# Kernel tuning notes

Hardware: AMD Instinct MI355X
Metric: run time of the kernel (lower is better)

The kernel has to match this reference:

```python
import jax, jax.numpy as jnp
import numpy as np

N_NODES = 50000
N_EDGES = 800000
IN_C = 116
HEADS = 4
OUT_C = 16
OUT_DIM = HEADS * OUT_C  # 64
NUM_GRAPHS = 100
NEG_SLOPE = 0.2
BN_EPS = 1e-5


def setup_inputs() -> dict:
    key = jax.random.key(0)
    ks = jax.random.split(key, 16)
    x = jax.random.normal(ks[0], (N_NODES, IN_C), dtype=jnp.float32)
    edge_index = jax.random.randint(ks[1], (2, N_EDGES), 0, N_NODES, dtype=jnp.int32)
    edge_attr = jax.random.normal(ks[2], (N_EDGES, 1), dtype=jnp.float32)
    batch = jnp.sort(jax.random.randint(ks[3], (N_NODES,), 0, NUM_GRAPHS, dtype=jnp.int32))
    s = 0.1
    return {
        "x": x, "edge_index": edge_index, "edge_attr": edge_attr, "batch": batch,
        "Wl": jax.random.normal(ks[4], (IN_C, OUT_DIM)) * s,
        "bl": jnp.zeros((OUT_DIM,), jnp.float32),
        "Wr": jax.random.normal(ks[5], (IN_C, OUT_DIM)) * s,
        "br": jnp.zeros((OUT_DIM,), jnp.float32),
        "We": jax.random.normal(ks[6], (1, OUT_DIM)) * s,
        "att": jax.random.normal(ks[7], (HEADS, OUT_C)) * s,
        "gat_bias": jnp.zeros((OUT_DIM,), jnp.float32),
        "gamma": jnp.ones((OUT_DIM,), jnp.float32),
        "beta": jnp.zeros((OUT_DIM,), jnp.float32),
        "Wres": jax.random.normal(ks[8], (IN_C, OUT_DIM)) * s,
        "bres": jnp.zeros((OUT_DIM,), jnp.float32),
        "W1": jax.random.normal(ks[9], (OUT_DIM, 64)) * s,
        "b1": jnp.zeros((64,), jnp.float32),
        "W2": jax.random.normal(ks[10], (64, 2)) * s,
        "b2": jnp.zeros((2,), jnp.float32),
    }


def _gatv2(x, edge_index, edge_attr, Wl, bl, Wr, br, We, att, gat_bias):
    N = x.shape[0]
    # linear transforms (PyG lin_l applies to source/message, lin_r to target)
    xl = (x @ Wl + bl).reshape(N, HEADS, OUT_C)
    xr = (x @ Wr + br).reshape(N, HEADS, OUT_C)
    # add self loops with fill_value=1.0 for edge_attr
    loops = jnp.arange(N, dtype=edge_index.dtype)
    src = jnp.concatenate([edge_index[0], loops])
    dst = jnp.concatenate([edge_index[1], loops])
    ea = jnp.concatenate([edge_attr, jnp.ones((N, 1), edge_attr.dtype)], axis=0)
    edge_emb = (ea @ We).reshape(-1, HEADS, OUT_C)          # [E+N, H, C]
    # GATv2 scores: att . leaky_relu(xl_j + xr_i + edge_emb)
    e = jax.nn.leaky_relu(xl[src] + xr[dst] + edge_emb, NEG_SLOPE)
    logits = jnp.einsum('ehc,hc->eh', e, att)                # [E+N, H]
    # segment softmax over incoming edges of each target node
    m = jax.ops.segment_max(logits, dst, num_segments=N)     # [N, H]
    ex = jnp.exp(logits - m[dst])
    denom = jax.ops.segment_sum(ex, dst, num_segments=N)     # [N, H]
    alpha = ex / denom[dst]
    # weighted scatter-add of source messages
    out = jax.ops.segment_sum(alpha[:, :, None] * xl[src], dst, num_segments=N)
    return out.reshape(N, OUT_DIM) + gat_bias


def reference(x, edge_index, edge_attr, batch, Wl, bl, Wr, br, We, att, gat_bias,
              gamma, beta, Wres, bres, W1, b1, W2, b2):
    h = _gatv2(x, edge_index, edge_attr, Wl, bl, Wr, br, We, att, gat_bias)
    # BatchNorm1d (training-style batch statistics over node dim)
    mu = jnp.mean(h, axis=0)
    var = jnp.var(h, axis=0)
    h = gamma * (h - mu) * jax.lax.rsqrt(var + BN_EPS) + beta
    # residual projection of original features
    h = h + (x @ Wres + bres)
    # global mean pool per graph
    sums = jax.ops.segment_sum(h, batch, num_segments=NUM_GRAPHS)
    cnts = jax.ops.segment_sum(jnp.ones((h.shape[0],), h.dtype), batch, num_segments=NUM_GRAPHS)
    pooled = sums / jnp.maximum(cnts, 1.0)[:, None]          # [G, 64]
    # 2-layer predictor with ReLU between
    z = jax.nn.relu(pooled @ W1 + b1)
    return z @ W2 + b2                                       # [G, 2]
```

## Files before the change

### kernel.cpp

```cpp
#include <hip/hip_runtime.h>
#include <hip/hip_bf16.h>

#define IN_C 116
#define HEADS 4
#define OUT_C 16
#define OUT_DIM 64
#define NEG_SLOPE 0.2f
#define BN_EPS 1e-5f
#define SCAN_B 256
#define LIN_BM 32
#define LIN_PAD 36

__global__ __launch_bounds__(256) void lin3_kernel(
    const float* __restrict__ x,
    const float* __restrict__ Wl, const float* __restrict__ bl,
    const float* __restrict__ Wr, const float* __restrict__ br,
    const float* __restrict__ Wres, const float* __restrict__ bres,
    float* __restrict__ xl, float* __restrict__ xr, float* __restrict__ xres,
    int N)
{
    __shared__ float xsT[IN_C * LIN_PAD];
    const int bn = blockIdx.x * LIN_BM;
    const int tid = threadIdx.x;

    for (int i = tid; i < LIN_BM * IN_C; i += 256) {
        int n = i / IN_C, k = i - n * IN_C;
        int gn = bn + n;
        xsT[k * LIN_PAD + n] = (gn < N) ? x[(size_t)gn * IN_C + k] : 0.f;
    }
    __syncthreads();

    const int j = tid & 63;
    const int t = tid >> 6;
    const int nbase = 8 * t;

    float al[8] = {0,0,0,0,0,0,0,0};
    float ar[8] = {0,0,0,0,0,0,0,0};
    float as_[8] = {0,0,0,0,0,0,0,0};

    #pragma unroll 4
    for (int k = 0; k < IN_C; ++k) {
        float4 xa = *(const float4*)&xsT[k * LIN_PAD + nbase];
        float4 xb = *(const float4*)&xsT[k * LIN_PAD + nbase + 4];
        float wl = Wl[k * OUT_DIM + j];
        float wr = Wr[k * OUT_DIM + j];
        float wsv = Wres[k * OUT_DIM + j];
        float xv[8] = {xa.x, xa.y, xa.z, xa.w, xb.x, xb.y, xb.z, xb.w};
        #pragma unroll
        for (int u = 0; u < 8; ++u) {
            al[u] += xv[u] * wl;
            ar[u] += xv[u] * wr;
            as_[u] += xv[u] * wsv;
        }
    }

    float blj = bl[j], brj = br[j], bsj = bres[j];
    #pragma unroll
    for (int u = 0; u < 8; ++u) {
        int gn = bn + nbase + u;
        if (gn < N) {
            xl[(size_t)gn * OUT_DIM + j]   = al[u] + blj;
            xr[(size_t)gn * OUT_DIM + j]   = ar[u] + brj;
            xres[(size_t)gn * OUT_DIM + j] = as_[u] + bsj;
        }
    }
}

__global__ __launch_bounds__(256) void deg_kernel(
    const int* __restrict__ ei, int* __restrict__ deg, int E, int Etot)
{
    int e = blockIdx.x * 256 + threadIdx.x;
    if (e >= Etot) return;
    int dst = (e < E) ? ei[E + e] : e - E;
    atomicAdd(&deg[dst], 1);
}

__global__ __launch_bounds__(SCAN_B) void scan1_kernel(
    const int* __restrict__ deg, int* __restrict__ rowcur,
    int* __restrict__ bsum, int N)
{
    __shared__ int ls[SCAN_B];
    int i = blockIdx.x * SCAN_B + threadIdx.x;
    int v = (i < N) ? deg[i] : 0;
    ls[threadIdx.x] = v;
    __syncthreads();
    for (int off = 1; off < SCAN_B; off <<= 1) {
        int add = (threadIdx.x >= off) ? ls[threadIdx.x - off] : 0;
        __syncthreads();
        ls[threadIdx.x] += add;
        __syncthreads();
    }
    if (i < N) rowcur[i] = ls[threadIdx.x] - v;
    if (threadIdx.x == SCAN_B - 1) bsum[blockIdx.x] = ls[SCAN_B - 1];
}

__global__ __launch_bounds__(SCAN_B) void scan2_kernel(int* __restrict__ bsum, int nb)
{
    __shared__ int ls[SCAN_B];
    int v = (threadIdx.x < nb) ? bsum[threadIdx.x] : 0;
    ls[threadIdx.x] = v;
    __syncthreads();
    for (int off = 1; off < SCAN_B; off <<= 1) {
        int add = (threadIdx.x >= off) ? ls[threadIdx.x - off] : 0;
        __syncthreads();
        ls[threadIdx.x] += add;
        __syncthreads();
    }
    if (threadIdx.x < nb) bsum[threadIdx.x] = ls[threadIdx.x] - v;
}

__global__ __launch_bounds__(256) void fill_kernel(
    const int* __restrict__ ei, const float* __restrict__ ea,
    int* __restrict__ rowcur, const int* __restrict__ bsum,
    int2* __restrict__ epack, int E, int Etot)
{
    int e = blockIdx.x * 256 + threadIdx.x;
    if (e >= Etot) return;
    int src, dst; float av;
    if (e < E) { src = ei[e]; dst = ei[E + e]; av = ea[e]; }
    else       { src = e - E; dst = e - E;    av = 1.0f; }
    int p = bsum[dst >> 8] + atomicAdd(&rowcur[dst], 1);
    epack[p] = make_int2(src, __float_as_int(av));
}

__global__ __launch_bounds__(256) void gat_gather_kernel(
    const int* __restrict__ rowcur, const int* __restrict__ bsum,
    const int2* __restrict__ epack,
    const float* __restrict__ xl, float* __restrict__ xr_hout,
    const float* __restrict__ We, const float* __restrict__ att,
    const float* __restrict__ gat_bias, int N)
{
    const int lane = threadIdx.x & 63;
    const int wv   = threadIdx.x >> 6;
    const int half = lane >> 5;
    const int c    = lane & 31;
    const int n = blockIdx.x * 8 + wv * 2 + half;
    if (n >= N) return;

    const float2 xr2 = *(const float2*)(xr_hout + (size_t)n * OUT_DIM + 2 * c);
    const float2 We2 = *(const float2*)(We + 2 * c);
    const float2 at2 = *(const float2*)(att + 2 * c);

    const int b = n >> 8;
    const int p1 = bsum[b] + rowcur[n];
    const int p0 = (n & 255) ? (bsum[b] + rowcur[n - 1]) : bsum[b];

    float den = 0.f, acc0 = 0.f, acc1 = 0.f;

#define EDGE_BODY(PP)                                                   \
    {                                                                   \
        int2 ep = epack[PP];                                            \
        int src = ep.x;                                                 \
        float av = __int_as_float(ep.y);                                \
        float2 xv = *(const float2*)(xl + (size_t)src * OUT_DIM + 2*c); \
        float s0 = xv.x + xr2.x + av * We2.x;                           \
        float s1 = xv.y + xr2.y + av * We2.y;                           \
        s0 = s0 > 0.f ? s0 : NEG_SLOPE * s0;                            \
        s1 = s1 > 0.f ? s1 : NEG_SLOPE * s1;                            \
        float pl = at2.x * s0 + at2.y * s1;                             \
        pl += __shfl_xor(pl, 1);                                        \
        pl += __shfl_xor(pl, 2);                                        \
        pl += __shfl_xor(pl, 4);                                        \
        float ex = __expf(pl);                                          \
        den += ex;                                                      \
        acc0 += ex * xv.x;                                              \
        acc1 += ex * xv.y;                                              \
    }

    int p = p0;
    while (p + 4 <= p1) {
        EDGE_BODY(p);
        EDGE_BODY(p + 1);
        EDGE_BODY(p + 2);
        EDGE_BODY(p + 3);
        p += 4;
    }
    while (p < p1) { EDGE_BODY(p); ++p; }
#undef EDGE_BODY

    const float2 bias2 = *(const float2*)(gat_bias + 2 * c);
    float inv = 1.0f / den;
    float2 o;
    o.x = acc0 * inv + bias2.x;
    o.y = acc1 * inv + bias2.y;
    *(float2*)(xr_hout + (size_t)n * OUT_DIM + 2 * c) = o;
}

__global__ __launch_bounds__(256) void stats_kernel(
    const float* __restrict__ h, float* __restrict__ chansum,
    float* __restrict__ chansumsq, int N)
{
    const int j = threadIdx.x & 63;
    const int t = threadIdx.x >> 6;
    float s = 0.f, ss = 0.f;
    for (int n = blockIdx.x * 4 + t; n < N; n += gridDim.x * 4) {
        float v = h[(size_t)n * OUT_DIM + j];
        s += v; ss += v * v;
    }
    __shared__ float ls[4][64], lss[4][64];
    ls[t][j] = s; lss[t][j] = ss;
    __syncthreads();
    if (t == 0) {
        atomicAdd(&chansum[j],   ls[0][j] + ls[1][j] + ls[2][j] + ls[3][j]);
        atomicAdd(&chansumsq[j], lss[0][j] + lss[1][j] + lss[2][j] + lss[3][j]);
    }
}

__global__ __launch_bounds__(256) void bn_res_pool_kernel(
    const float* __restrict__ hraw, const float* __restrict__ xres,
    const float* __restrict__ chansum, const float* __restrict__ chansumsq,
    const float* __restrict__ gamma, const float* __restrict__ beta,
    const int* __restrict__ batch,
    float* __restrict__ pooled, float* __restrict__ cnt, int N)
{
    const int j = threadIdx.x & 63;
    const int t = threadIdx.x >> 6;
    const int base = blockIdx.x * 256;
    const float invN = 1.0f / (float)N;
    const float mj = chansum[j] * invN;
    const float var = chansumsq[j] * invN - mj * mj;
    const float rj = rsqrtf(var + BN_EPS);
    const float gj = gamma[j], bj = beta[j];

    float sum = 0.f, c = 0.f;
    int gcur = -1;
    for (int i = t; i < 256; i += 4) {
        int n = base + i;
        if (n >= N) break;
        int g = batch[n];
        if (g != gcur) {
            if (gcur >= 0) {
                atomicAdd(&pooled[gcur * OUT_DIM + j], sum);
                if (j == 0) atomicAdd(&cnt[gcur], c);
            }
            sum = 0.f; c = 0.f; gcur = g;
        }
        float v = gj * (hraw[(size_t)n * OUT_DIM + j] - mj) * rj + bj
                + xres[(size_t)n * OUT_DIM + j];
        sum += v; c += 1.f;
    }
    if (gcur >= 0) {
        atomicAdd(&pooled[gcur * OUT_DIM + j], sum);
        if (j == 0) atomicAdd(&cnt[gcur], c);
    }
}

__global__ __launch_bounds__(64) void mlp_kernel(
    const float* __restrict__ pooled, const float* __restrict__ cnt,
    const float* __restrict__ W1, const float* __restrict__ b1,
    const float* __restrict__ W2, const float* __restrict__ b2,
    float* __restrict__ out, int G)
{
    int g = blockIdx.x, j = threadIdx.x;
    __shared__ float ps[64];
    float c = cnt[g];
    c = c > 1.0f ? c : 1.0f;
    ps[j] = pooled[g * OUT_DIM + j] / c;
    __syncthreads();
    float z = b1[j];
    for (int k = 0; k < 64; ++k) z += ps[k] * W1[k * 64 + j];
    z = z > 0.f ? z : 0.f;
    float o0 = z * W2[j * 2 + 0];
    float o1 = z * W2[j * 2 + 1];
    #pragma unroll
    for (int off = 32; off > 0; off >>= 1) {
        o0 += __shfl_down(o0, off);
        o1 += __shfl_down(o1, off);
    }
    if (j == 0) {
        out[g * 2 + 0] = o0 + b2[0];
        out[g * 2 + 1] = o1 + b2[1];
    }
}

extern "C" void kernel_launch(void* const* d_in, const int* in_sizes, int n_in,
                              void* d_out, int out_size, void* d_ws, size_t ws_size,
                              hipStream_t stream) {
    const float* x        = (const float*)d_in[0];
    const int*   ei       = (const int*)d_in[1];
    const float* ea       = (const float*)d_in[2];
    const int*   batch    = (const int*)d_in[3];
    const float* Wl       = (const float*)d_in[4];
    const float* bl       = (const float*)d_in[5];
    const float* Wr       = (const float*)d_in[6];
    const float* br       = (const float*)d_in[7];
    const float* We       = (const float*)d_in[8];
    const float* att      = (const float*)d_in[9];
    const float* gat_bias = (const float*)d_in[10];
    const float* gamma    = (const float*)d_in[11];
    const float* beta     = (const float*)d_in[12];
    const float* Wres     = (const float*)d_in[13];
    const float* bres     = (const float*)d_in[14];
    const float* W1       = (const float*)d_in[15];
    const float* b1       = (const float*)d_in[16];
    const float* W2       = (const float*)d_in[17];
    const float* b2       = (const float*)d_in[18];
    float* out = (float*)d_out;

    const int N = in_sizes[0] / IN_C;
    const int E = in_sizes[1] / 2;
    const int G = out_size / 2;
    const int Etot = E + N;

    float* ws = (float*)d_ws;
    float* xl      = ws;
    float* xr      = xl + (size_t)N * OUT_DIM;
    float* xres    = xr + (size_t)N * OUT_DIM;
    int2*  epack   = (int2*)(xres + (size_t)N * OUT_DIM);
    int*   rowcur  = (int*)(epack + Etot);
    int*   bsum    = rowcur + N;
    int*   deg     = bsum + 256;
    float* chansum   = (float*)(deg + N);
    float* chansumsq = chansum + 64;
    float* pooled    = chansumsq + 64;
    float* cnt       = pooled + (size_t)G * OUT_DIM;

    size_t zero_bytes = (size_t)((char*)(cnt + G) - (char*)deg);
    hipMemsetAsync(deg, 0, zero_bytes, stream);

    const int nb = (N + SCAN_B - 1) / SCAN_B;

    lin3_kernel<<<(N + LIN_BM - 1) / LIN_BM, 256, 0, stream>>>(
        x, Wl, bl, Wr, br, Wres, bres, xl, xr, xres, N);

    deg_kernel<<<(Etot + 255) / 256, 256, 0, stream>>>(ei, deg, E, Etot);
    scan1_kernel<<<nb, SCAN_B, 0, stream>>>(deg, rowcur, bsum, N);
    scan2_kernel<<<1, SCAN_B, 0, stream>>>(bsum, nb);
    fill_kernel<<<(Etot + 255) / 256, 256, 0, stream>>>(
        ei, ea, rowcur, bsum, epack, E, Etot);

    gat_gather_kernel<<<(N + 7) / 8, 256, 0, stream>>>(
        rowcur, bsum, epack, xl, xr, We, att, gat_bias, N);

    stats_kernel<<<256, 256, 0, stream>>>(xr, chansum, chansumsq, N);

    bn_res_pool_kernel<<<(N + 255) / 256, 256, 0, stream>>>(
        xr, xres, chansum, chansumsq, gamma, beta, batch, pooled, cnt, N);

    mlp_kernel<<<G, 64, 0, stream>>>(pooled, cnt, W1, b1, W2, b2, out, G);
}
```

Baseline: 327.8 us.

## Fold degree count into linear kernel, handle self-loops implicitly, widen gather lanes

The edge-degree atomics move into the tail of the fused linear-projection kernel, so the separate degree launch goes away. Self-loop edges are no longer built into the CSR arrays. Instead each node's self term is computed directly at the start of the gather, which shrinks the degree, fill and epack work by N entries. The gather now gives each node 16 lanes with float4 loads instead of 32 lanes with float2, fitting 4 nodes per wavefront and needing one fewer shuffle step per reduction. The trade-off is more registers per lane and less parallelism across lanes within each node's edge loop.

```diff
diff --git a/kernel.cpp b/kernel.cpp
--- a/kernel.cpp
+++ b/kernel.cpp
@@ -11,12 +11,13 @@
 #define LIN_BM 32
 #define LIN_PAD 36
 
-__global__ __launch_bounds__(256) void lin3_kernel(
+__global__ __launch_bounds__(256) void lin3_deg_kernel(
     const float* __restrict__ x,
     const float* __restrict__ Wl, const float* __restrict__ bl,
     const float* __restrict__ Wr, const float* __restrict__ br,
     const float* __restrict__ Wres, const float* __restrict__ bres,
     float* __restrict__ xl, float* __restrict__ xr, float* __restrict__ xres,
+    const int* __restrict__ ei, int* __restrict__ deg, int E,
     int N)
 {
     __shared__ float xsT[IN_C * LIN_PAD];
@@ -64,15 +65,10 @@
             xres[(size_t)gn * OUT_DIM + j] = as_[u] + bsj;
         }
     }
-}
-
-__global__ __launch_bounds__(256) void deg_kernel(
-    const int* __restrict__ ei, int* __restrict__ deg, int E, int Etot)
-{
-    int e = blockIdx.x * 256 + threadIdx.x;
-    if (e >= Etot) return;
-    int dst = (e < E) ? ei[E + e] : e - E;
-    atomicAdd(&deg[dst], 1);
+
+    const int stride = gridDim.x * 256;
+    for (int e = blockIdx.x * 256 + tid; e < E; e += stride)
+        atomicAdd(&deg[ei[E + e]], 1);
 }
 
 __global__ __launch_bounds__(SCAN_B) void scan1_kernel(
@@ -112,13 +108,13 @@
 __global__ __launch_bounds__(256) void fill_kernel(
     const int* __restrict__ ei, const float* __restrict__ ea,
     int* __restrict__ rowcur, const int* __restrict__ bsum,
-    int2* __restrict__ epack, int E, int Etot)
+    int2* __restrict__ epack, int E)
 {
     int e = blockIdx.x * 256 + threadIdx.x;
-    if (e >= Etot) return;
-    int src, dst; float av;
-    if (e < E) { src = ei[e]; dst = ei[E + e]; av = ea[e]; }
-    else       { src = e - E; dst = e - E;    av = 1.0f; }
+    if (e >= E) return;
+    int src = ei[e];
+    int dst = ei[E + e];
+    float av = ea[e];
     int p = bsum[dst >> 8] + atomicAdd(&rowcur[dst], 1);
     epack[p] = make_int2(src, __float_as_int(av));
 }
@@ -132,39 +128,61 @@
 {
     const int lane = threadIdx.x & 63;
     const int wv   = threadIdx.x >> 6;
-    const int half = lane >> 5;
-    const int c    = lane & 31;
-    const int n = blockIdx.x * 8 + wv * 2 + half;
+    const int g    = lane >> 4;
+    const int q    = lane & 15;
+    const int n = blockIdx.x * 16 + wv * 4 + g;
     if (n >= N) return;
 
-    const float2 xr2 = *(const float2*)(xr_hout + (size_t)n * OUT_DIM + 2 * c);
-    const float2 We2 = *(const float2*)(We + 2 * c);
-    const float2 at2 = *(const float2*)(att + 2 * c);
+    const float4 xr4 = *(const float4*)(xr_hout + (size_t)n * OUT_DIM + 4 * q);
+    const float4 We4 = *(const float4*)(We + 4 * q);
+    const float4 at4 = *(const float4*)(att + 4 * q);
 
     const int b = n >> 8;
     const int p1 = bsum[b] + rowcur[n];
     const int p0 = (n & 255) ? (bsum[b] + rowcur[n - 1]) : bsum[b];
 
-    float den = 0.f, acc0 = 0.f, acc1 = 0.f;
+    float den, acc0, acc1, acc2, acc3;
+    {
+        float4 xv = *(const float4*)(xl + (size_t)n * OUT_DIM + 4 * q);
+        float s0 = xv.x + xr4.x + We4.x;
+        float s1 = xv.y + xr4.y + We4.y;
+        float s2 = xv.z + xr4.z + We4.z;
+        float s3 = xv.w + xr4.w + We4.w;
+        s0 = s0 > 0.f ? s0 : NEG_SLOPE * s0;
+        s1 = s1 > 0.f ? s1 : NEG_SLOPE * s1;
+        s2 = s2 > 0.f ? s2 : NEG_SLOPE * s2;
+        s3 = s3 > 0.f ? s3 : NEG_SLOPE * s3;
+        float pl = at4.x * s0 + at4.y * s1 + at4.z * s2 + at4.w * s3;
+        pl += __shfl_xor(pl, 1);
+        pl += __shfl_xor(pl, 2);
+        float ex = __expf(pl);
+        den = ex;
+        acc0 = ex * xv.x; acc1 = ex * xv.y; acc2 = ex * xv.z; acc3 = ex * xv.w;
+    }
 
 #define EDGE_BODY(PP)                                                   \
     {                                                                   \
         int2 ep = epack[PP];                                            \
         int src = ep.x;                                                 \
         float av = __int_as_float(ep.y);                                \
-        float2 xv = *(const float2*)(xl + (size_t)src * OUT_DIM + 2*c); \
-        float s0 = xv.x + xr2.x + av * We2.x;                           \
-        float s1 = xv.y + xr2.y + av * We2.y;                           \
+        float4 xv = *(const float4*)(xl + (size_t)src * OUT_DIM + 4*q); \
+        float s0 = xv.x + xr4.x + av * We4.x;                           \
+        float s1 = xv.y + xr4.y + av * We4.y;                           \
+        float s2 = xv.z + xr4.z + av * We4.z;                           \
+        float s3 = xv.w + xr4.w + av * We4.w;                           \
         s0 = s0 > 0.f ? s0 : NEG_SLOPE * s0;                            \
         s1 = s1 > 0.f ? s1 : NEG_SLOPE * s1;                            \
-        float pl = at2.x * s0 + at2.y * s1;                             \
+        s2 = s2 > 0.f ? s2 : NEG_SLOPE * s2;                            \
+        s3 = s3 > 0.f ? s3 : NEG_SLOPE * s3;                            \
+        float pl = at4.x * s0 + at4.y * s1 + at4.z * s2 + at4.w * s3;   \
         pl += __shfl_xor(pl, 1);                                        \
         pl += __shfl_xor(pl, 2);                                        \
-        pl += __shfl_xor(pl, 4);                                        \
         float ex = __expf(pl);                                          \
         den += ex;                                                      \
         acc0 += ex * xv.x;                                              \
         acc1 += ex * xv.y;                                              \
+        acc2 += ex * xv.z;                                              \
+        acc3 += ex * xv.w;                                              \
     }
 
     int p = p0;
@@ -178,12 +196,14 @@
     while (p < p1) { EDGE_BODY(p); ++p; }
 #undef EDGE_BODY
 
-    const float2 bias2 = *(const float2*)(gat_bias + 2 * c);
+    const float4 bias4 = *(const float4*)(gat_bias + 4 * q);
     float inv = 1.0f / den;
-    float2 o;
-    o.x = acc0 * inv + bias2.x;
-    o.y = acc1 * inv + bias2.y;
-    *(float2*)(xr_hout + (size_t)n * OUT_DIM + 2 * c) = o;
+    float4 o;
+    o.x = acc0 * inv + bias4.x;
+    o.y = acc1 * inv + bias4.y;
+    o.z = acc2 * inv + bias4.z;
+    o.w = acc3 * inv + bias4.w;
+    *(float4*)(xr_hout + (size_t)n * OUT_DIM + 4 * q) = o;
 }
 
 __global__ __launch_bounds__(256) void stats_kernel(
@@ -300,14 +320,13 @@
     const int N = in_sizes[0] / IN_C;
     const int E = in_sizes[1] / 2;
     const int G = out_size / 2;
-    const int Etot = E + N;
 
     float* ws = (float*)d_ws;
     float* xl      = ws;
     float* xr      = xl + (size_t)N * OUT_DIM;
     float* xres    = xr + (size_t)N * OUT_DIM;
     int2*  epack   = (int2*)(xres + (size_t)N * OUT_DIM);
-    int*   rowcur  = (int*)(epack + Etot);
+    int*   rowcur  = (int*)(epack + E);
     int*   bsum    = rowcur + N;
     int*   deg     = bsum + 256;
     float* chansum   = (float*)(deg + N);
@@ -320,16 +339,15 @@
 
     const int nb = (N + SCAN_B - 1) / SCAN_B;
 
-    lin3_kernel<<<(N + LIN_BM - 1) / LIN_BM, 256, 0, stream>>>(
-        x, Wl, bl, Wr, br, Wres, bres, xl, xr, xres, N);
-
-    deg_kernel<<<(Etot + 255) / 256, 256, 0, stream>>>(ei, deg, E, Etot);
+    lin3_deg_kernel<<<(N + LIN_BM - 1) / LIN_BM, 256, 0, stream>>>(
+        x, Wl, bl, Wr, br, Wres, bres, xl, xr, xres, ei, deg, E, N);
+
     scan1_kernel<<<nb, SCAN_B, 0, stream>>>(deg, rowcur, bsum, N);
     scan2_kernel<<<1, SCAN_B, 0, stream>>>(bsum, nb);
-    fill_kernel<<<(Etot + 255) / 256, 256, 0, stream>>>(
-        ei, ea, rowcur, bsum, epack, E, Etot);
-
-    gat_gather_kernel<<<(N + 7) / 8, 256, 0, stream>>>(
+    fill_kernel<<<(E + 255) / 256, 256, 0, stream>>>(
+        ei, ea, rowcur, bsum, epack, E);
+
+    gat_gather_kernel<<<(N + 15) / 16, 256, 0, stream>>>(
         rowcur, bsum, epack, xl, xr, We, att, gat_bias, N);
 
     stats_kernel<<<256, 256, 0, stream>>>(xr, chansum, chansumsq, N);
```

After: 315.5 us. 1.04x faster.
